# Kernel optimization log

Measured on AMD Instinct MI355X. Metric: run time of the kernel, lower is better.

The kernel has to match this reference:

```python
import jax, jax.numpy as jnp
import numpy as np
from jax import lax

B, L, D = 4, 2048, 2048
R = 2048          # max_rank (== d_model so the original torch code's final add is shape-valid)
DH = D // 4       # gate MLP hidden


def setup_inputs() -> dict:
    key = jax.random.key(0)
    ks = jax.random.split(key, 12)
    s = 0.02
    x = jax.random.normal(ks[0], (B, L, D), dtype=jnp.float32)
    # nn.Linear weights are (out_features, in_features)
    Wu = jax.random.normal(ks[1], (R, D), dtype=jnp.float32) * s
    bu = jnp.zeros((R,), dtype=jnp.float32)
    Wv = jax.random.normal(ks[2], (R, D), dtype=jnp.float32) * s
    bv = jnp.zeros((R,), dtype=jnp.float32)
    Wg1 = jax.random.normal(ks[3], (DH, D), dtype=jnp.float32) * s
    bg1 = jnp.zeros((DH,), dtype=jnp.float32)
    Wg2 = jax.random.normal(ks[4], (R, DH), dtype=jnp.float32) * s
    bg2 = jnp.zeros((R,), dtype=jnp.float32)
    # depthwise Conv1d(d_model, d_model, k=3, groups=d_model): weight (D, 1, 3)
    conv_w = jax.random.normal(ks[5], (D, 1, 3), dtype=jnp.float32) * s
    conv_b = jnp.zeros((D,), dtype=jnp.float32)
    return {"x": x, "Wu": Wu, "bu": bu, "Wv": Wv, "bv": bv,
            "Wg1": Wg1, "bg1": bg1, "Wg2": Wg2, "bg2": bg2,
            "conv_w": conv_w, "conv_b": conv_b}


def reference(x, Wu, bu, Wv, bv, Wg1, bg1, Wg2, bg2, conv_w, conv_b):
    # depthwise conv over sequence: T term
    xc = jnp.transpose(x, (0, 2, 1))                      # (B, D, L)
    t = lax.conv_general_dilated(
        xc, conv_w, window_strides=(1,), padding=[(1, 1)],
        dimension_numbers=("NCH", "OIH", "NCH"),
        feature_group_count=D)
    t_out = jnp.transpose(t + conv_b[None, :, None], (0, 2, 1))  # (B, L, D)

    u = jnp.einsum("bld,rd->blr", x, Wu) + bu             # (B, L, R)
    v = jnp.einsum("bld,rd->blr", x, Wv) + bv             # (B, L, R)
    h = jax.nn.relu(jnp.einsum("bld,hd->blh", x, Wg1) + bg1)
    gates = jax.nn.sigmoid(jnp.einsum("blh,rh->blr", h, Wg2) + bg2)

    u_gated = u * gates
    v_gated = v * gates
    k_cumsum = jnp.cumsum(u_gated, axis=1)                # prefix-scan over seq
    global_out = k_cumsum * v_gated                       # (B, L, R)
    # matches torch: global_out @ U_proj.weight.t()[:max_rank, :]
    uv_term = jnp.einsum("blr,rd->bld", global_out, Wu.T[:R, :])
    return t_out + uv_term
```

## Files before the change

kernel.cpp:

```cpp
#include <hip/hip_runtime.h>
#include <hip/hip_bf16.h>
#include <math.h>

typedef __bf16 bf16;
typedef __attribute__((ext_vector_type(8))) __bf16 bf16x8;
typedef __attribute__((ext_vector_type(4))) __bf16 bf16x4;
typedef __attribute__((ext_vector_type(4))) float f32x4;

#define B_  4
#define L_  2048
#define D_  2048
#define R_  2048
#define DH_ 512
#define M_  (B_ * L_)

__device__ __forceinline__ void gload16(const void* g, void* l) {
    __builtin_amdgcn_global_load_lds(
        (__attribute__((address_space(1))) void*)(uintptr_t)g,
        (__attribute__((address_space(3))) void*)l,
        16, 0, 0);
}

__device__ __forceinline__ int swz(int r, int cu) {
    return r * 64 + (((cu ^ (r >> 1)) & 3) << 4);
}

__global__ void k_cvt(const float* __restrict__ in, bf16* __restrict__ out, int n4) {
    int i = blockIdx.x * blockDim.x + threadIdx.x;
    if (i >= n4) return;
    float4 v = reinterpret_cast<const float4*>(in)[i];
    bf16x4 o = { (bf16)v.x, (bf16)v.y, (bf16)v.z, (bf16)v.w };
    reinterpret_cast<bf16x4*>(out)[i] = o;
}

__global__ void k_conv(const float* __restrict__ x, const float* __restrict__ w,
                       const float* __restrict__ cb, float* __restrict__ out) {
    int idx = blockIdx.x * blockDim.x + threadIdx.x;
    int dq = idx & (D_/4 - 1);
    int bl = idx >> 9;
    int l  = bl & (L_ - 1);
    int d0 = dq * 4;
    const float4* xp = reinterpret_cast<const float4*>(x);
    float4 xc = xp[idx];
    float4 xm = (l > 0)      ? xp[idx - D_/4] : make_float4(0.f,0.f,0.f,0.f);
    float4 xq = (l < L_ - 1) ? xp[idx + D_/4] : make_float4(0.f,0.f,0.f,0.f);
    const float* pm = (const float*)&xm;
    const float* pc = (const float*)&xc;
    const float* pq = (const float*)&xq;
    float4 r;
    float* pr = (float*)&r;
    #pragma unroll
    for (int j = 0; j < 4; ++j) {
        int d = d0 + j;
        pr[j] = pm[j]*w[d*3+0] + pc[j]*w[d*3+1] + pq[j]*w[d*3+2] + cb[d];
    }
    reinterpret_cast<float4*>(out)[idx] = r;
}

template<int EPI>
__global__ __launch_bounds__(512, 2)
void k_gemm2(const bf16* __restrict__ A, const bf16* __restrict__ W,
             const float* __restrict__ bias, bf16* __restrict__ ob,
             float* __restrict__ of, int N, int K)
{
    __shared__ __align__(16) char lds[98304];
    const int t    = threadIdx.x;
    const int lane = t & 63;
    const int w8   = t >> 6;
    const int wr   = w8 >> 2;
    const int wc   = w8 & 3;
    const int bm   = blockIdx.y, bn = blockIdx.x;
    const bf16* Ab = A + (size_t)bm * 256 * K;
    const bf16* Wb = W + (size_t)bn * 256 * K;
    const int NT = K >> 5;

    const int sr0 = t >> 2;
    const int sc  = t & 3;
    const int scc = (sc ^ (sr0 >> 1)) & 3;
    const int fr  = lane & 15;
    const int cu  = lane >> 4;
    const int wbase = w8 << 10;

    const bf16* gaB = Ab + (size_t)sr0 * K + scc * 8;
    const bf16* gbB = Wb + (size_t)sr0 * K + scc * 8;

    f32x4 acc[8][4] = {};

    {
        char* A0 = lds;          char* B0 = lds + 16384;
        char* A1 = lds + 32768;  char* B1 = lds + 49152;
        const bf16* ga = gaB;  const bf16* gb = gbB;
        gload16(ga,                   A0 + wbase);
        gload16(ga + (size_t)128 * K, A0 + 8192 + wbase);
        gload16(gb,                   B0 + wbase);
        gload16(gb + (size_t)128 * K, B0 + 8192 + wbase);
        int t1 = (NT > 1) ? 1 : 0;
        ga = gaB + t1 * 32;  gb = gbB + t1 * 32;
        gload16(ga,                   A1 + wbase);
        gload16(ga + (size_t)128 * K, A1 + 8192 + wbase);
        gload16(gb,                   B1 + wbase);
        gload16(gb + (size_t)128 * K, B1 + 8192 + wbase);
    }
    asm volatile("s_waitcnt vmcnt(4)" ::: "memory");
    __builtin_amdgcn_s_barrier();

    int cur = 0;
    for (int tt = 0; tt < NT; ++tt) {
        const char* Al = lds + cur * 32768;
        const char* Bl = Al + 16384;
        int nb = cur + 2; if (nb >= 3) nb -= 3;
        int ts = tt + 2; if (ts >= NT) ts = NT - 1;
        char* An = lds + nb * 32768;
        char* Bn = An + 16384;
        const bf16* ga = gaB + ts * 32;
        const bf16* gb = gbB + ts * 32;

        bf16x8 bfrag[4], afrag[4];

        #pragma unroll
        for (int n = 0; n < 4; ++n)
            bfrag[n] = *(const bf16x8*)(Bl + swz(wc*64 + n*16 + fr, cu));
        #pragma unroll
        for (int g = 0; g < 4; ++g)
            afrag[g] = *(const bf16x8*)(Al + swz(wr*128 + g*16 + fr, cu));
        gload16(ga,                   An + wbase);
        gload16(ga + (size_t)128 * K, An + 8192 + wbase);
        __builtin_amdgcn_s_barrier();
        __builtin_amdgcn_s_setprio(1);
        #pragma unroll
        for (int g = 0; g < 4; ++g)
            #pragma unroll
            for (int n = 0; n < 4; ++n)
                acc[g][n] = __builtin_amdgcn_mfma_f32_16x16x32_bf16(
                    afrag[g], bfrag[n], acc[g][n], 0, 0, 0);
        __builtin_amdgcn_s_setprio(0);
        __builtin_amdgcn_s_barrier();

        #pragma unroll
        for (int g = 0; g < 4; ++g)
            afrag[g] = *(const bf16x8*)(Al + swz(wr*128 + 64 + g*16 + fr, cu));
        gload16(gb,                   Bn + wbase);
        gload16(gb + (size_t)128 * K, Bn + 8192 + wbase);
        __builtin_amdgcn_s_barrier();
        __builtin_amdgcn_s_setprio(1);
        #pragma unroll
        for (int g = 0; g < 4; ++g)
            #pragma unroll
            for (int n = 0; n < 4; ++n)
                acc[4+g][n] = __builtin_amdgcn_mfma_f32_16x16x32_bf16(
                    afrag[g], bfrag[n], acc[4+g][n], 0, 0, 0);
        __builtin_amdgcn_s_setprio(0);
        asm volatile("s_waitcnt vmcnt(4)" ::: "memory");
        __builtin_amdgcn_s_barrier();

        cur = cur + 1; if (cur >= 3) cur -= 3;
    }

    const int fq = lane >> 4;
    #pragma unroll
    for (int g = 0; g < 8; ++g) {
        #pragma unroll
        for (int n = 0; n < 4; ++n) {
            const int row0 = bm*256 + wr*128 + g*16 + fq*4;
            const int col  = bn*256 + wc*64 + n*16 + fr;
            float bb = (EPI == 3) ? 0.f : bias[col];
            #pragma unroll
            for (int j = 0; j < 4; ++j) {
                float v = acc[g][n][j] + bb;
                size_t o = (size_t)(row0 + j) * N + col;
                if      (EPI == 0) ob[o] = (bf16)v;
                else if (EPI == 2) ob[o] = (bf16)(1.f / (1.f + __expf(-v)));
                else               of[o] = of[o] + v;
            }
        }
    }
}

template<int EPI>
__global__ __launch_bounds__(256)
void k_gemm(const bf16* __restrict__ A, const bf16* __restrict__ W,
            const float* __restrict__ bias, bf16* __restrict__ ob,
            float* __restrict__ of, int N, int K)
{
    __shared__ __align__(16) bf16 As[128 * 32];
    __shared__ __align__(16) bf16 Bs[128 * 32];
    const int t    = threadIdx.x;
    const int lane = t & 63;
    const int wv   = t >> 6;
    const int wr   = wv >> 1, wc = wv & 1;
    const int bm   = blockIdx.y, bn = blockIdx.x;
    const bf16* Ab = A + (size_t)bm * 128 * K;
    const bf16* Wb = W + (size_t)bn * 128 * K;
    const int r0 = t >> 2;
    const int kq = (t & 3) * 8;
    char* ldsA = (char*)As + wv * 1024;
    char* ldsB = (char*)Bs + wv * 1024;

    f32x4 acc[4][4] = {};
    const int fr = lane & 15;
    const int fk = (lane >> 4) * 8;

    for (int kt = 0; kt < K; kt += 32) {
        const bf16* ak = Ab + (size_t)r0 * K + kt + kq;
        const bf16* wk = Wb + (size_t)r0 * K + kt + kq;
        gload16(ak,                 ldsA);
        gload16(ak + (size_t)64*K,  ldsA + 4096);
        gload16(wk,                 ldsB);
        gload16(wk + (size_t)64*K,  ldsB + 4096);
        __syncthreads();
        bf16x8 af[4], bw[4];
        #pragma unroll
        for (int i = 0; i < 4; ++i) {
            af[i] = *(const bf16x8*)&As[(wr*64 + i*16 + fr) * 32 + fk];
            bw[i] = *(const bf16x8*)&Bs[(wc*64 + i*16 + fr) * 32 + fk];
        }
        #pragma unroll
        for (int mi = 0; mi < 4; ++mi)
            #pragma unroll
            for (int ni = 0; ni < 4; ++ni)
                acc[mi][ni] = __builtin_amdgcn_mfma_f32_16x16x32_bf16(
                    af[mi], bw[ni], acc[mi][ni], 0, 0, 0);
        __syncthreads();
    }

    const int fq = lane >> 4;
    #pragma unroll
    for (int mi = 0; mi < 4; ++mi) {
        #pragma unroll
        for (int ni = 0; ni < 4; ++ni) {
            const int row0 = bm*128 + wr*64 + mi*16 + fq*4;
            const int col  = bn*128 + wc*64 + ni*16 + fr;
            float bb = bias[col];
            #pragma unroll
            for (int j = 0; j < 4; ++j) {
                float v = acc[mi][ni][j] + bb;
                size_t o = (size_t)(row0 + j) * N + col;
                ob[o] = (bf16)fmaxf(v, 0.f);
            }
        }
    }
}

__global__ void k_scan_sum(const bf16* __restrict__ U, const bf16* __restrict__ G,
                           float* __restrict__ CS) {
    int idx = blockIdx.x * blockDim.x + threadIdx.x;
    int r  = idx & (R_ - 1);
    int ch = (idx >> 11) & 15;
    int b  = idx >> 15;
    size_t base = ((size_t)(b * L_ + ch * 128)) * R_ + r;
    float s = 0.f;
    #pragma unroll 8
    for (int i = 0; i < 128; ++i) {
        float u = (float)U[base + (size_t)i * R_];
        float g = (float)G[base + (size_t)i * R_];
        s = fmaf(u, g, s);
    }
    CS[idx] = s;
}

__global__ void k_scan_apply(const bf16* __restrict__ U, const bf16* __restrict__ V,
                             const bf16* __restrict__ G, const float* __restrict__ CS,
                             bf16* __restrict__ GB) {
    int idx = blockIdx.x * blockDim.x + threadIdx.x;
    int r  = idx & (R_ - 1);
    int ch = (idx >> 11) & 15;
    int b  = idx >> 15;
    float run = 0.f;
    for (int c = 0; c < ch; ++c)
        run += CS[(((b << 4) + c) << 11) + r];
    size_t base = ((size_t)(b * L_ + ch * 128)) * R_ + r;
    #pragma unroll 4
    for (int i = 0; i < 128; ++i) {
        size_t o = base + (size_t)i * R_;
        float u = (float)U[o];
        float g = (float)G[o];
        float v = (float)V[o];
        run = fmaf(u, g, run);
        GB[o] = (bf16)(run * v * g);
    }
}

extern "C" void kernel_launch(void* const* d_in, const int* in_sizes, int n_in,
                              void* d_out, int out_size, void* d_ws, size_t ws_size,
                              hipStream_t stream)
{
    const float* x   = (const float*)d_in[0];
    const float* Wu  = (const float*)d_in[1];
    const float* bu  = (const float*)d_in[2];
    const float* Wv  = (const float*)d_in[3];
    const float* bv  = (const float*)d_in[4];
    const float* Wg1 = (const float*)d_in[5];
    const float* bg1 = (const float*)d_in[6];
    const float* Wg2 = (const float*)d_in[7];
    const float* bg2 = (const float*)d_in[8];
    const float* cw  = (const float*)d_in[9];
    const float* cb  = (const float*)d_in[10];
    float* out = (float*)d_out;

    char* w = (char*)d_ws;
    bf16* xb   = (bf16*)w;  w += (size_t)M_ * D_  * 2;
    bf16* Wub  = (bf16*)w;  w += (size_t)R_ * D_  * 2;
    bf16* Wvb  = (bf16*)w;  w += (size_t)R_ * D_  * 2;
    bf16* Wg1b = (bf16*)w;  w += (size_t)DH_* D_  * 2;
    bf16* Wg2b = (bf16*)w;  w += (size_t)R_ * DH_ * 2;
    bf16* U    = (bf16*)w;  w += (size_t)M_ * R_  * 2;
    bf16* V    = (bf16*)w;  w += (size_t)M_ * R_  * 2;
    bf16* H    = (bf16*)w;  w += (size_t)M_ * DH_ * 2;
    bf16* GT   = (bf16*)w;  w += (size_t)M_ * R_  * 2;
    bf16* GB   = (bf16*)w;  w += (size_t)M_ * R_  * 2;
    float* CS  = (float*)w; w += (size_t)B_ * 16 * R_ * 4;

    k_cvt<<<M_*D_/4/256,  256, 0, stream>>>(x,   xb,   M_*D_/4);
    k_cvt<<<R_*D_/4/256,  256, 0, stream>>>(Wu,  Wub,  R_*D_/4);
    k_cvt<<<R_*D_/4/256,  256, 0, stream>>>(Wv,  Wvb,  R_*D_/4);
    k_cvt<<<DH_*D_/4/256, 256, 0, stream>>>(Wg1, Wg1b, DH_*D_/4);
    k_cvt<<<R_*DH_/4/256, 256, 0, stream>>>(Wg2, Wg2b, R_*DH_/4);

    k_conv<<<M_*D_/4/256, 256, 0, stream>>>(x, cw, cb, out);

    k_gemm2<0><<<dim3(R_/256,  M_/256), 512, 0, stream>>>(xb, Wub,  bu,  U,  nullptr, R_,  D_);
    k_gemm2<0><<<dim3(R_/256,  M_/256), 512, 0, stream>>>(xb, Wvb,  bv,  V,  nullptr, R_,  D_);
    k_gemm<1> <<<dim3(DH_/128, M_/128), 256, 0, stream>>>(xb, Wg1b, bg1, H,  nullptr, DH_, D_);
    k_gemm2<2><<<dim3(R_/256,  M_/256), 512, 0, stream>>>(H,  Wg2b, bg2, GT, nullptr, R_,  DH_);

    k_scan_sum  <<<B_*16*R_/256, 256, 0, stream>>>(U, GT, CS);
    k_scan_apply<<<B_*16*R_/256, 256, 0, stream>>>(U, V, GT, CS, GB);

    k_gemm2<3><<<dim3(D_/256, M_/256), 512, 0, stream>>>(GB, Wub, nullptr, nullptr, out, D_, R_);
}
```

Before: 567.3 us.

## Deepen GEMM LDS pipeline to four stages and remap blocks for XCD locality

Grows the GEMM LDS ring from three to four 32 KB stages, prefetching three K-tiles ahead. The two half-iterations with separate barriers become one iteration that loads all eight A fragments and issues all MFMAs together. Block IDs are remapped so blocks on the same XCD share nearby A/W tiles for better L2 reuse. The cost is more LDS per block (128 KB, which may lower occupancy below the launch bound of 2), more live fragment registers, and a remap that hardcodes an 8-column, 32-row grid.

```diff
diff --git a/kernel.cpp b/kernel.cpp
--- a/kernel.cpp
+++ b/kernel.cpp
@@ -63,13 +63,19 @@
              const float* __restrict__ bias, bf16* __restrict__ ob,
              float* __restrict__ of, int N, int K)
 {
-    __shared__ __align__(16) char lds[98304];
+    __shared__ __align__(16) char lds[131072];
     const int t    = threadIdx.x;
     const int lane = t & 63;
     const int w8   = t >> 6;
     const int wr   = w8 >> 2;
     const int wc   = w8 & 3;
-    const int bm   = blockIdx.y, bn = blockIdx.x;
+
+    const int lid  = blockIdx.y * 8 + blockIdx.x;
+    const int xcd  = lid & 7;
+    const int slot = lid >> 3;
+    const int bn   = (xcd & 1) * 4 + (slot & 3);
+    const int bm   = (xcd >> 1) * 8 + (slot >> 2);
+
     const bf16* Ab = A + (size_t)bm * 256 * K;
     const bf16* Wb = W + (size_t)bn * 256 * K;
     const int NT = K >> 5;
@@ -86,74 +92,54 @@
 
     f32x4 acc[8][4] = {};
 
-    {
-        char* A0 = lds;          char* B0 = lds + 16384;
-        char* A1 = lds + 32768;  char* B1 = lds + 49152;
-        const bf16* ga = gaB;  const bf16* gb = gbB;
-        gload16(ga,                   A0 + wbase);
-        gload16(ga + (size_t)128 * K, A0 + 8192 + wbase);
-        gload16(gb,                   B0 + wbase);
-        gload16(gb + (size_t)128 * K, B0 + 8192 + wbase);
-        int t1 = (NT > 1) ? 1 : 0;
-        ga = gaB + t1 * 32;  gb = gbB + t1 * 32;
-        gload16(ga,                   A1 + wbase);
-        gload16(ga + (size_t)128 * K, A1 + 8192 + wbase);
-        gload16(gb,                   B1 + wbase);
-        gload16(gb + (size_t)128 * K, B1 + 8192 + wbase);
-    }
-    asm volatile("s_waitcnt vmcnt(4)" ::: "memory");
+    #pragma unroll
+    for (int p = 0; p < 3; ++p) {
+        char* Abuf = lds + p * 32768;
+        char* Bbuf = Abuf + 16384;
+        const bf16* ga = gaB + p * 32;
+        const bf16* gb = gbB + p * 32;
+        gload16(ga,                   Abuf + wbase);
+        gload16(ga + (size_t)128 * K, Abuf + 8192 + wbase);
+        gload16(gb,                   Bbuf + wbase);
+        gload16(gb + (size_t)128 * K, Bbuf + 8192 + wbase);
+    }
+    asm volatile("s_waitcnt vmcnt(8)" ::: "memory");
     __builtin_amdgcn_s_barrier();
 
-    int cur = 0;
     for (int tt = 0; tt < NT; ++tt) {
-        const char* Al = lds + cur * 32768;
+        const char* Al = lds + (tt & 3) * 32768;
         const char* Bl = Al + 16384;
-        int nb = cur + 2; if (nb >= 3) nb -= 3;
-        int ts = tt + 2; if (ts >= NT) ts = NT - 1;
-        char* An = lds + nb * 32768;
+        char* An = lds + ((tt + 3) & 3) * 32768;
         char* Bn = An + 16384;
+        int ts = tt + 3; if (ts >= NT) ts = NT - 1;
         const bf16* ga = gaB + ts * 32;
         const bf16* gb = gbB + ts * 32;
 
-        bf16x8 bfrag[4], afrag[4];
-
+        bf16x8 bfrag[4], afrag[8];
         #pragma unroll
         for (int n = 0; n < 4; ++n)
             bfrag[n] = *(const bf16x8*)(Bl + swz(wc*64 + n*16 + fr, cu));
         #pragma unroll
-        for (int g = 0; g < 4; ++g)
+        for (int g = 0; g < 8; ++g)
             afrag[g] = *(const bf16x8*)(Al + swz(wr*128 + g*16 + fr, cu));
+
         gload16(ga,                   An + wbase);
         gload16(ga + (size_t)128 * K, An + 8192 + wbase);
+        gload16(gb,                   Bn + wbase);
+        gload16(gb + (size_t)128 * K, Bn + 8192 + wbase);
+
+        asm volatile("s_waitcnt vmcnt(8)" ::: "memory");
         __builtin_amdgcn_s_barrier();
+
         __builtin_amdgcn_s_setprio(1);
         #pragma unroll
-        for (int g = 0; g < 4; ++g)
+        for (int g = 0; g < 8; ++g)
             #pragma unroll
             for (int n = 0; n < 4; ++n)
                 acc[g][n] = __builtin_amdgcn_mfma_f32_16x16x32_bf16(
                     afrag[g], bfrag[n], acc[g][n], 0, 0, 0);
         __builtin_amdgcn_s_setprio(0);
         __builtin_amdgcn_s_barrier();
-
-        #pragma unroll
-        for (int g = 0; g < 4; ++g)
-            afrag[g] = *(const bf16x8*)(Al + swz(wr*128 + 64 + g*16 + fr, cu));
-        gload16(gb,                   Bn + wbase);
-        gload16(gb + (size_t)128 * K, Bn + 8192 + wbase);
-        __builtin_amdgcn_s_barrier();
-        __builtin_amdgcn_s_setprio(1);
-        #pragma unroll
-        for (int g = 0; g < 4; ++g)
-            #pragma unroll
-            for (int n = 0; n < 4; ++n)
-                acc[4+g][n] = __builtin_amdgcn_mfma_f32_16x16x32_bf16(
-                    afrag[g], bfrag[n], acc[4+g][n], 0, 0, 0);
-        __builtin_amdgcn_s_setprio(0);
-        asm volatile("s_waitcnt vmcnt(4)" ::: "memory");
-        __builtin_amdgcn_s_barrier();
-
-        cur = cur + 1; if (cur >= 3) cur -= 3;
     }
 
     const int fq = lane >> 4;
```

Result: faster. 556.1 us (-2.0%).
